# Kernel optimization log

Measured on AMD Instinct MI355X. Metric: run time of the kernel, lower is better.

The kernel has to match this reference:

```python
import jax, jax.numpy as jnp
import numpy as np

B, N, L, C = 4, 16, 192, 64
H = 128
ROW, COL = 16, 12  # L == ROW*COL, ROW >= COL
NUM = 2  # class_num


def setup_inputs() -> dict:
    key = jax.random.key(0)
    ks = jax.random.split(key, 12)
    s = 1.0 / np.sqrt(H).astype(np.float32)
    u = lambda k, shape: jax.random.uniform(k, shape, jnp.float32, -s, s)
    return {
        "x": jax.random.normal(ks[0], (B, N, L, C), jnp.float32),
        "pad_mask": jnp.ones((B, N), jnp.bool_),
        "fc3_w": u(ks[1], (H, C)), "fc3_b": u(ks[2], (H,)),
        "fc4_w": u(ks[3], (H, H)), "fc4_b": u(ks[4], (H,)),
        "W_enc": u(ks[5], (NUM, 6 * H, 3 * H)), "B_enc": u(ks[6], (NUM, 6 * H)),
        "fc1_w": u(ks[7], (NUM, 1, H)), "fc1_b": u(ks[8], (NUM, 1)),
        "fc2_w": u(ks[9], (NUM, 1, H)), "fc2_b": u(ks[10], (NUM, 1)),
    }


def _witran_encoder(a, W, Bb):
    # a: [COL*BN, slice_len, H] diagonally-shifted input; W: [6H, 3H]; Bb: [6H]
    RBN, slice_len, _ = a.shape
    BN = RBN // COL
    R = COL  # Water2sea_slice_num (after permute(2,0,1,3), slices run over col)
    slice_ids = jnp.arange(RBN) // BN
    xs = jnp.transpose(a, (1, 0, 2))  # [slice_len, RBN, H]

    def step(carry, inp):
        h_row, h_col = carry
        x_s, s = inp
        g = jnp.concatenate([h_row, h_col, x_s], axis=-1) @ W.T  # [RBN, 6H]
        # torch adds bias only to first batch*(s+1) rows, and only while s < slice_num
        mask = (slice_ids <= s) & (s < R)
        g = g + jnp.where(mask[:, None], Bb, jnp.zeros((), g.dtype))
        sig = jax.nn.sigmoid(g[:, : 4 * H])
        th = jnp.tanh(g[:, 4 * H:])
        u_r, o_r, u_c, o_c = jnp.split(sig, 4, axis=-1)
        i_r, i_c = jnp.split(th, 2, axis=-1)
        h_row = jnp.tanh((1 - u_r) * h_row + u_r * i_r) * o_r
        h_col = jnp.tanh((1 - u_c) * h_col + u_c * i_c) * o_c
        # saved pieces (only valid for late s; we keep the last, which is always valid)
        loc = jnp.clip(s - ROW + 1, 0, R - 1)
        row_save = jax.lax.dynamic_slice_in_dim(h_row, loc * BN, BN, axis=0)
        col_save = h_col[(R - 1) * BN:, :]  # save BEFORE roll, as in torch
        h_col = jnp.roll(h_col, BN, axis=0)
        return (h_row, h_col), (row_save, col_save)

    h0 = jnp.zeros((RBN, H), a.dtype)
    (_, _), (row_saves, col_saves) = jax.lax.scan(
        step, (h0, h0), (xs, jnp.arange(slice_len)))
    # last entries == hidden_row_all[:, -1, -1, :], hidden_col_all[:, -1, -1, :]
    return row_saves[-1], col_saves[-1]  # each [BN, H]


def reference(x, pad_mask, fc3_w, fc3_b, fc4_w, fc4_b, W_enc, B_enc,
              fc1_w, fc1_b, fc2_w, fc2_b):
    Bn, Nn = x.shape[0], x.shape[1]
    h = jax.nn.relu(x @ fc3_w.T + fc3_b) @ fc4_w.T + fc4_b  # [B,N,L,H]
    xr = h.reshape(-1, ROW, COL, H)          # [BN, row, col, H]
    inp = jnp.transpose(xr, (2, 0, 1, 3))    # [col, BN, row, H]
    slice_len = COL + ROW - 1
    # diagonal 'water2sea' shift: transfer[r, :, r:r+ROW] = inp[r]
    padded = jnp.pad(inp, ((0, 0), (0, 0), (0, COL - 1), (0, 0)))
    transfer = jax.vmap(lambda t, r: jnp.roll(t, r, axis=1))(padded, jnp.arange(COL))
    a = transfer.reshape(COL * Bn * Nn, slice_len, H)

    def per_class(W, Bb, f1w, f1b, f2w, f2b):
        row_last, col_last = _witran_encoder(a, W, Bb)
        # torch: row := hidden_col_all tail, col := hidden_row_all tail
        out = 0.5 * (col_last @ f1w.T + f1b) + 0.5 * (row_last @ f2w.T + f2b)
        return out[:, 0]  # [BN]

    y = jax.vmap(per_class)(W_enc, B_enc, fc1_w, fc1_b, fc2_w, fc2_b)  # [NUM, BN]
    return jnp.transpose(y).reshape(Bn, Nn, NUM)
```

## Files before the change

### kernel.cpp

```cpp
#include <hip/hip_runtime.h>

typedef _Float16 hf;
typedef _Float16 half2v __attribute__((ext_vector_type(2)));
typedef _Float16 half8 __attribute__((ext_vector_type(8)));
typedef float f32x4 __attribute__((ext_vector_type(4)));
typedef int int4v __attribute__((ext_vector_type(4)));

constexpr int Steps = 27;

constexpr int OFF_WX = 393216;
constexpr int OFF_F3 = 589824;
constexpr int OFF_F4 = 598016;
constexpr int OFF_XW = 614400;

__device__ __forceinline__ int aidx(int r, int k) {
  int blk = k >> 3;
  return r * 256 + (((blk ^ (r & 7)) & 31) << 3) + (k & 7);
}
__device__ __forceinline__ int hidx(int r, int k) {
  int blk = k >> 3;
  return r * 128 + (((blk ^ (r & 15)) & 15) << 3) + (k & 7);
}
__device__ __forceinline__ int xidx(int r, int k) {
  int blk = k >> 3;
  return r * 64 + (((blk ^ (r & 7)) & 7) << 3) + (k & 7);
}
__device__ __forceinline__ float rcpf_(float x) { return __builtin_amdgcn_rcpf(x); }
__device__ __forceinline__ float sigmoidf_(float x) { return rcpf_(1.0f + __expf(-x)); }
__device__ __forceinline__ float tanh_(float x) { return 1.0f - 2.0f * rcpf_(__expf(2.0f * x) + 1.0f); }

__device__ __forceinline__ void bar_lgkm() {
  __builtin_amdgcn_sched_barrier(0);
  asm volatile("s_waitcnt lgkmcnt(0)");
  __builtin_amdgcn_s_barrier();
  __builtin_amdgcn_sched_barrier(0);
}

__global__ __launch_bounds__(512) void prep(const float* __restrict__ fc3_w,
                                            const float* __restrict__ fc4_w,
                                            const float* __restrict__ W_enc,
                                            hf* __restrict__ wsh) {
  int idx = blockIdx.x * 512 + threadIdx.x;
  if (idx >= OFF_XW) return;
  float v;
  if (idx < OFF_WX) {
    int jj = idx & 7, lane = (idx >> 3) & 63, rest = idx >> 9;
    int ks = rest & 7; rest >>= 3;
    int j = rest % 3; rest /= 3;
    int wv = rest & 15, cls = rest >> 4;
    int gate = (wv < 8) ? (j < 2 ? j : 4) : (j < 2 ? j + 2 : 5);
    int n = gate * 128 + (wv & 7) * 16 + (lane & 15);
    int k = ks * 32 + ((lane >> 4) << 3) + jj;
    v = W_enc[(cls * 768 + n) * 384 + k];
  } else if (idx < OFF_F3) {
    int f = idx - OFF_WX;
    int j = f & 7, lane = (f >> 3) & 63, rest = f >> 9;
    int ks = rest & 3; rest >>= 2;
    int wv = rest & 7; rest >>= 3;
    int gate = rest % 6, cls = rest / 6;
    int n = gate * 128 + wv * 16 + (lane & 15);
    int k = 256 + ks * 32 + ((lane >> 4) << 3) + j;
    v = W_enc[(cls * 768 + n) * 384 + k];
  } else if (idx < OFF_F4) {
    int f = idx - OFF_F3;
    int j = f & 7, lane = (f >> 3) & 63, rest = f >> 9;
    int ks = rest & 1, wv = rest >> 1;
    int n = wv * 16 + (lane & 15), k = ks * 32 + ((lane >> 4) << 3) + j;
    v = fc3_w[n * 64 + k];
  } else {
    int f = idx - OFF_F4;
    int j = f & 7, lane = (f >> 3) & 63, rest = f >> 9;
    int ks = rest & 3, wv = rest >> 2;
    int n = wv * 16 + (lane & 15), k = ks * 32 + ((lane >> 4) << 3) + j;
    v = fc4_w[n * 128 + k];
  }
  wsh[idx] = (hf)v;
}

__global__ __launch_bounds__(512) void prelude(
    const float* __restrict__ x, const float* __restrict__ fc3_b, const float* __restrict__ fc4_b,
    const float* __restrict__ B_enc, const hf* __restrict__ wsh, hf* __restrict__ xWb) {
  const int t = threadIdx.x, lane = t & 63, wv = t >> 6;
  const int c16 = lane & 15, quad = lane >> 4;
  const int row0 = blockIdx.x * 64, bn = row0 / 192, l0 = row0 % 192;
  const int d = wv * 16 + c16;

  __shared__ __attribute__((aligned(16))) hf xA[64 * 64];
  __shared__ __attribute__((aligned(16))) hf hbuf[64 * 128];
  __shared__ __attribute__((aligned(16))) hf xout[64 * 768];
  __shared__ float actf[64];

  {
    int r = t >> 3, cb = (t & 7) * 8;
    const float* xp = x + (size_t)(row0 + r) * 64 + cb;
    f32x4 a = *(const f32x4*)xp, b = *(const f32x4*)(xp + 4);
    half8 h;
    h[0] = (hf)a.x; h[1] = (hf)a.y; h[2] = (hf)a.z; h[3] = (hf)a.w;
    h[4] = (hf)b.x; h[5] = (hf)b.y; h[6] = (hf)b.z; h[7] = (hf)b.w;
    *(half8*)&xA[xidx(r, cb)] = h;
  }
  if (t < 64) {
    int l = l0 + t;
    actf[t] = ((l / 12) + (l % 12)) < 12 ? 1.f : 0.f;
  }
  __syncthreads();

  {
    float b3v = fc3_b[d];
    half8 w0 = *(const half8*)(wsh + OFF_F3 + (wv * 2 + 0) * 512 + lane * 8);
    half8 w1 = *(const half8*)(wsh + OFF_F3 + (wv * 2 + 1) * 512 + lane * 8);
    f32x4 acc[4] = {{0, 0, 0, 0}, {0, 0, 0, 0}, {0, 0, 0, 0}, {0, 0, 0, 0}};
#pragma unroll
    for (int mt = 0; mt < 4; ++mt) {
      half8 a0 = *(const half8*)&xA[xidx(mt * 16 + c16, quad * 8)];
      half8 a1 = *(const half8*)&xA[xidx(mt * 16 + c16, 32 + quad * 8)];
      acc[mt] = __builtin_amdgcn_mfma_f32_16x16x32_f16(a0, w0, acc[mt], 0, 0, 0);
      acc[mt] = __builtin_amdgcn_mfma_f32_16x16x32_f16(a1, w1, acc[mt], 0, 0, 0);
    }
#pragma unroll
    for (int mt = 0; mt < 4; ++mt)
#pragma unroll
      for (int r = 0; r < 4; ++r)
        hbuf[hidx(mt * 16 + quad * 4 + r, d)] = (hf)fmaxf(acc[mt][r] + b3v, 0.f);
  }
  __syncthreads();

  {
    float b4v = fc4_b[d];
    half8 w4[4];
#pragma unroll
    for (int ks = 0; ks < 4; ++ks)
      w4[ks] = *(const half8*)(wsh + OFF_F4 + (wv * 4 + ks) * 512 + lane * 8);
    f32x4 acc[4] = {{0, 0, 0, 0}, {0, 0, 0, 0}, {0, 0, 0, 0}, {0, 0, 0, 0}};
#pragma unroll
    for (int mt = 0; mt < 4; ++mt)
#pragma unroll
      for (int ks = 0; ks < 4; ++ks) {
        half8 a = *(const half8*)&hbuf[hidx(mt * 16 + c16, ks * 32 + quad * 8)];
        acc[mt] = __builtin_amdgcn_mfma_f32_16x16x32_f16(a, w4[ks], acc[mt], 0, 0, 0);
      }
    __syncthreads();
#pragma unroll
    for (int mt = 0; mt < 4; ++mt)
#pragma unroll
      for (int r = 0; r < 4; ++r)
        hbuf[hidx(mt * 16 + quad * 4 + r, d)] = (hf)(acc[mt][r] + b4v);
  }
  __syncthreads();

  half8 af[4][4];
#pragma unroll
  for (int mt = 0; mt < 4; ++mt)
#pragma unroll
    for (int ks = 0; ks < 4; ++ks)
      af[mt][ks] = *(const half8*)&hbuf[hidx(mt * 16 + c16, ks * 32 + quad * 8)];

  for (int cls = 0; cls < 2; ++cls) {
    for (int g = 0; g < 6; ++g) {
      int pos = (g < 2) ? g : (g < 4 ? g + 1 : (g == 4 ? 2 : 5));
      half8 wf[4];
#pragma unroll
      for (int ks = 0; ks < 4; ++ks)
        wf[ks] = *(const half8*)(wsh + OFF_WX + (((cls * 6 + g) * 8 + wv) * 4 + ks) * 512 + lane * 8);
      float bv = B_enc[cls * 768 + g * 128 + d];
#pragma unroll
      for (int mt = 0; mt < 4; ++mt) {
        f32x4 acc = {0.f, 0.f, 0.f, 0.f};
#pragma unroll
        for (int ks = 0; ks < 4; ++ks)
          acc = __builtin_amdgcn_mfma_f32_16x16x32_f16(af[mt][ks], wf[ks], acc, 0, 0, 0);
#pragma unroll
        for (int r = 0; r < 4; ++r) {
          int row = mt * 16 + quad * 4 + r;
          xout[row * 768 + d * 6 + pos] = (hf)(acc[r] + actf[row] * bv);
        }
      }
    }
    __syncthreads();
    {
      const int* src = (const int*)xout;
      int* dst = (int*)(xWb + (((size_t)cls * 64 + bn) * 192 + l0) * 768);
#pragma unroll
      for (int i = 0; i < 12; ++i) {
        int base = (t + i * 512) * 4;
        *(int4v*)&dst[base] = *(const int4v*)&src[base];
      }
    }
    __syncthreads();
  }
}

__device__ __forceinline__ float lo16f(unsigned v) {
  return (float)__builtin_bit_cast(half2v, v)[0];
}
__device__ __forceinline__ float hi16f(unsigned v) {
  return (float)__builtin_bit_cast(half2v, v)[1];
}

__global__ __launch_bounds__(512, 2) __attribute__((amdgpu_waves_per_eu(2, 2))) void witran(
    const hf* __restrict__ wsh, const float* __restrict__ fc1_w, const float* __restrict__ fc1_b,
    const float* __restrict__ fc2_w, const float* __restrict__ fc2_b,
    const hf* __restrict__ xWb, float* __restrict__ out) {
  const int cls = blockIdx.x & 1, bn = blockIdx.x >> 1;
  const int t = threadIdx.x, lane = t & 63, wv = t >> 6;
  const int c16 = lane & 15, quad = lane >> 4;
  const int d = wv * 16 + c16;
  const bool act = (quad < 3);
  const int c0 = quad * 4;

  __shared__ __attribute__((aligned(16))) hf wlds[8 * 4096];
  __shared__ __attribute__((aligned(16))) hf A[2][4096];
  __shared__ float red[128];

  for (int i = t; i < 4096; i += 512) ((int*)A)[i] = 0;

  half8 wf[5][8];
  {
    const hf* wbR = wsh + ((size_t)((cls * 16 + wv) * 3) * 8) * 512 + lane * 8;
    const hf* wbC = wsh + ((size_t)((cls * 16 + 8 + wv) * 3) * 8) * 512 + lane * 8;
#pragma unroll
    for (int j = 0; j < 3; ++j)
#pragma unroll
      for (int ks = 0; ks < 8; ++ks)
        wf[j][ks] = *(const half8*)(wbR + (j * 8 + ks) * 512);
#pragma unroll
    for (int j = 0; j < 2; ++j)
#pragma unroll
      for (int ks = 0; ks < 8; ++ks)
        wf[3 + j][ks] = *(const half8*)(wbC + (j * 8 + ks) * 512);
#pragma unroll
    for (int ks = 0; ks < 8; ++ks)
      *(half8*)&wlds[wv * 4096 + ks * 512 + lane * 8] = *(const half8*)(wbC + (16 + ks) * 512);
  }

  const hf* xg = xWb + ((size_t)cls * 64 + bn) * 192 * 768;
  int xrun = d * 12 - c0 * 16896;
  unsigned pxc[4][3];
  float hr[4] = {0.f, 0.f, 0.f, 0.f};

  auto xload = [&](int s) {
#pragma unroll
    for (int r = 0; r < 4; ++r) {
      int c = c0 + r;
      bool ok = act && ((unsigned)(s - c) < 16u);
      int off = ok ? (xrun - r * 16896) : 0;
      const hf* p = (const hf*)((const char*)xg + off);
      pxc[r][0] = *(const unsigned*)p;
      pxc[r][1] = *(const unsigned*)(p + 2);
      pxc[r][2] = *(const unsigned*)(p + 4);
    }
    xrun += 18432;
  };

  auto step = [&](const hf* Ac, hf* An, int s) {
    float hcold[4];
#pragma unroll
    for (int r = 0; r < 4; ++r) hcold[r] = (float)Ac[aidx(c0 + r, 128 + d)];
    f32x4 acc[6];
#pragma unroll
    for (int g = 0; g < 6; ++g) acc[g] = (f32x4){0.f, 0.f, 0.f, 0.f};
#pragma unroll
    for (int ks = 0; ks < 8; ++ks) {
      half8 av = *(const half8*)&Ac[aidx(c16, ks * 32 + quad * 8)];
#pragma unroll
      for (int g = 0; g < 5; ++g)
        acc[g] = __builtin_amdgcn_mfma_f32_16x16x32_f16(av, wf[g][ks], acc[g], 0, 0, 0);
      half8 w5 = *(const half8*)&wlds[wv * 4096 + ks * 512 + lane * 8];
      acc[5] = __builtin_amdgcn_mfma_f32_16x16x32_f16(av, w5, acc[5], 0, 0, 0);
    }
    if (act) {
#pragma unroll
      for (int r = 0; r < 4; ++r) {
        int c = c0 + r;
        bool okx = ((unsigned)(s - c) < 16u);
        unsigned v0 = okx ? pxc[r][0] : 0u;
        unsigned v1 = okx ? pxc[r][1] : 0u;
        unsigned v2 = okx ? pxc[r][2] : 0u;
        float xur = lo16f(v0), xor_ = hi16f(v0);
        float xir = lo16f(v1), xuc = hi16f(v1);
        float xoc = lo16f(v2), xic = hi16f(v2);
        float uu = sigmoidf_(acc[0][r] + xur);
        float oo = sigmoidf_(acc[1][r] + xor_);
        float ii = tanh_(acc[2][r] + xir);
        float h1 = tanh_(hr[r] + uu * (ii - hr[r])) * oo;
        hr[r] = h1;
        An[aidx(c, d)] = (hf)h1;
        float u2 = sigmoidf_(acc[3][r] + xuc);
        float o2 = sigmoidf_(acc[4][r] + xoc);
        float i2 = tanh_(acc[5][r] + xic);
        float h2 = tanh_(hcold[r] + u2 * (i2 - hcold[r])) * o2;
        int cw = (c == 11) ? 0 : c + 1;
        An[aidx(cw, 128 + d)] = (hf)h2;
      }
    }
    xload(s + 1);
    bar_lgkm();
  };

  xload(0);
  bar_lgkm();

#pragma unroll 1
  for (int s = 0; s < Steps - 1; s += 2) {
    step(A[0], A[1], s);
    step(A[1], A[0], s + 1);
  }
  step(A[0], A[1], Steps - 1);

  const hf* Af = A[1];
  if (t < 128) {
    float hrv = (float)Af[aidx(11, t)];
    float hcv = (float)Af[aidx(0, 128 + t)];
    red[t] = 0.5f * (hcv * fc1_w[cls * 128 + t] + hrv * fc2_w[cls * 128 + t]);
  }
  __syncthreads();
  if (t == 0) {
    float sum = 0.f;
    for (int i = 0; i < 128; ++i) sum += red[i];
    out[bn * 2 + cls] = sum + 0.5f * (fc1_b[cls] + fc2_b[cls]);
  }
}

extern "C" void kernel_launch(void* const* d_in, const int* in_sizes, int n_in,
                              void* d_out, int out_size, void* d_ws, size_t ws_size,
                              hipStream_t stream) {
  const float* x = (const float*)d_in[0];
  const float* fc3_w = (const float*)d_in[2];
  const float* fc3_b = (const float*)d_in[3];
  const float* fc4_w = (const float*)d_in[4];
  const float* fc4_b = (const float*)d_in[5];
  const float* W_enc = (const float*)d_in[6];
  const float* B_enc = (const float*)d_in[7];
  const float* fc1_w = (const float*)d_in[8];
  const float* fc1_b = (const float*)d_in[9];
  const float* fc2_w = (const float*)d_in[10];
  const float* fc2_b = (const float*)d_in[11];
  float* out = (float*)d_out;

  hf* wsh = (hf*)d_ws;
  hf* xWb = wsh + OFF_XW;

  prep<<<dim3(1200), dim3(512), 0, stream>>>(fc3_w, fc4_w, W_enc, wsh);
  prelude<<<dim3(192), dim3(512), 0, stream>>>(x, fc3_b, fc4_b, B_enc, wsh, xWb);
  witran<<<dim3(128), dim3(512), 0, stream>>>(wsh, fc1_w, fc1_b, fc2_w, fc2_b, xWb, out);
}
```

Before: 161.7 us.

## Drop weight prep kernel and gather fp32 weights directly; halve prelude tile

Removes the separate prep kernel that reformatted fc3, fc4 and W_enc into fp16 MFMA-fragment layout. Each consumer kernel now loads fp32 weights straight from the original tensors and converts them in registers. The prelude tile shrinks from 64 to 32 rows, doubling its grid to 384 blocks for better CU coverage. This saves one launch and one pass over the weights, but the per-thread fp32 loads are strided and less coalesced, and weight bytes are re-read by more blocks.

```diff
diff --git a/kernel.cpp b/kernel.cpp
--- a/kernel.cpp
+++ b/kernel.cpp
@@ -2,16 +2,12 @@
 
 typedef _Float16 hf;
 typedef _Float16 half2v __attribute__((ext_vector_type(2)));
+typedef _Float16 half4 __attribute__((ext_vector_type(4)));
 typedef _Float16 half8 __attribute__((ext_vector_type(8)));
 typedef float f32x4 __attribute__((ext_vector_type(4)));
 typedef int int4v __attribute__((ext_vector_type(4)));
 
 constexpr int Steps = 27;
-
-constexpr int OFF_WX = 393216;
-constexpr int OFF_F3 = 589824;
-constexpr int OFF_F4 = 598016;
-constexpr int OFF_XW = 614400;
 
 __device__ __forceinline__ int aidx(int r, int k) {
   int blk = k >> 3;
@@ -36,70 +32,36 @@
   __builtin_amdgcn_sched_barrier(0);
 }
 
-__global__ __launch_bounds__(512) void prep(const float* __restrict__ fc3_w,
-                                            const float* __restrict__ fc4_w,
-                                            const float* __restrict__ W_enc,
-                                            hf* __restrict__ wsh) {
-  int idx = blockIdx.x * 512 + threadIdx.x;
-  if (idx >= OFF_XW) return;
-  float v;
-  if (idx < OFF_WX) {
-    int jj = idx & 7, lane = (idx >> 3) & 63, rest = idx >> 9;
-    int ks = rest & 7; rest >>= 3;
-    int j = rest % 3; rest /= 3;
-    int wv = rest & 15, cls = rest >> 4;
-    int gate = (wv < 8) ? (j < 2 ? j : 4) : (j < 2 ? j + 2 : 5);
-    int n = gate * 128 + (wv & 7) * 16 + (lane & 15);
-    int k = ks * 32 + ((lane >> 4) << 3) + jj;
-    v = W_enc[(cls * 768 + n) * 384 + k];
-  } else if (idx < OFF_F3) {
-    int f = idx - OFF_WX;
-    int j = f & 7, lane = (f >> 3) & 63, rest = f >> 9;
-    int ks = rest & 3; rest >>= 2;
-    int wv = rest & 7; rest >>= 3;
-    int gate = rest % 6, cls = rest / 6;
-    int n = gate * 128 + wv * 16 + (lane & 15);
-    int k = 256 + ks * 32 + ((lane >> 4) << 3) + j;
-    v = W_enc[(cls * 768 + n) * 384 + k];
-  } else if (idx < OFF_F4) {
-    int f = idx - OFF_F3;
-    int j = f & 7, lane = (f >> 3) & 63, rest = f >> 9;
-    int ks = rest & 1, wv = rest >> 1;
-    int n = wv * 16 + (lane & 15), k = ks * 32 + ((lane >> 4) << 3) + j;
-    v = fc3_w[n * 64 + k];
-  } else {
-    int f = idx - OFF_F4;
-    int j = f & 7, lane = (f >> 3) & 63, rest = f >> 9;
-    int ks = rest & 3, wv = rest >> 2;
-    int n = wv * 16 + (lane & 15), k = ks * 32 + ((lane >> 4) << 3) + j;
-    v = fc4_w[n * 128 + k];
-  }
-  wsh[idx] = (hf)v;
+__device__ __forceinline__ half8 gather8(const float* __restrict__ p) {
+  f32x4 a = *(const f32x4*)p, b = *(const f32x4*)(p + 4);
+  half8 h;
+  h[0] = (hf)a.x; h[1] = (hf)a.y; h[2] = (hf)a.z; h[3] = (hf)a.w;
+  h[4] = (hf)b.x; h[5] = (hf)b.y; h[6] = (hf)b.z; h[7] = (hf)b.w;
+  return h;
 }
 
 __global__ __launch_bounds__(512) void prelude(
-    const float* __restrict__ x, const float* __restrict__ fc3_b, const float* __restrict__ fc4_b,
-    const float* __restrict__ B_enc, const hf* __restrict__ wsh, hf* __restrict__ xWb) {
+    const float* __restrict__ x, const float* __restrict__ fc3_w, const float* __restrict__ fc3_b,
+    const float* __restrict__ fc4_w, const float* __restrict__ fc4_b,
+    const float* __restrict__ W_enc, const float* __restrict__ B_enc, hf* __restrict__ xWb) {
   const int t = threadIdx.x, lane = t & 63, wv = t >> 6;
   const int c16 = lane & 15, quad = lane >> 4;
-  const int row0 = blockIdx.x * 64, bn = row0 / 192, l0 = row0 % 192;
+  const int row0 = blockIdx.x * 32, bn = row0 / 192, l0 = row0 % 192;
   const int d = wv * 16 + c16;
 
-  __shared__ __attribute__((aligned(16))) hf xA[64 * 64];
-  __shared__ __attribute__((aligned(16))) hf hbuf[64 * 128];
-  __shared__ __attribute__((aligned(16))) hf xout[64 * 768];
-  __shared__ float actf[64];
+  __shared__ __attribute__((aligned(16))) hf xA[32 * 64];
+  __shared__ __attribute__((aligned(16))) hf hbuf[32 * 128];
+  __shared__ __attribute__((aligned(16))) hf xout[32 * 768];
+  __shared__ float actf[32];
 
   {
-    int r = t >> 3, cb = (t & 7) * 8;
-    const float* xp = x + (size_t)(row0 + r) * 64 + cb;
-    f32x4 a = *(const f32x4*)xp, b = *(const f32x4*)(xp + 4);
-    half8 h;
+    int r = t >> 4, cb = (t & 15) * 4;
+    f32x4 a = *(const f32x4*)(x + (size_t)(row0 + r) * 64 + cb);
+    half4 h;
     h[0] = (hf)a.x; h[1] = (hf)a.y; h[2] = (hf)a.z; h[3] = (hf)a.w;
-    h[4] = (hf)b.x; h[5] = (hf)b.y; h[6] = (hf)b.z; h[7] = (hf)b.w;
-    *(half8*)&xA[xidx(r, cb)] = h;
-  }
-  if (t < 64) {
+    *(half4*)&xA[xidx(r, cb)] = h;
+  }
+  if (t < 32) {
     int l = l0 + t;
     actf[t] = ((l / 12) + (l % 12)) < 12 ? 1.f : 0.f;
   }
@@ -107,18 +69,18 @@
 
   {
     float b3v = fc3_b[d];
-    half8 w0 = *(const half8*)(wsh + OFF_F3 + (wv * 2 + 0) * 512 + lane * 8);
-    half8 w1 = *(const half8*)(wsh + OFF_F3 + (wv * 2 + 1) * 512 + lane * 8);
-    f32x4 acc[4] = {{0, 0, 0, 0}, {0, 0, 0, 0}, {0, 0, 0, 0}, {0, 0, 0, 0}};
-#pragma unroll
-    for (int mt = 0; mt < 4; ++mt) {
+    half8 w0 = gather8(fc3_w + d * 64 + quad * 8);
+    half8 w1 = gather8(fc3_w + d * 64 + 32 + quad * 8);
+    f32x4 acc[2] = {{0, 0, 0, 0}, {0, 0, 0, 0}};
+#pragma unroll
+    for (int mt = 0; mt < 2; ++mt) {
       half8 a0 = *(const half8*)&xA[xidx(mt * 16 + c16, quad * 8)];
       half8 a1 = *(const half8*)&xA[xidx(mt * 16 + c16, 32 + quad * 8)];
       acc[mt] = __builtin_amdgcn_mfma_f32_16x16x32_f16(a0, w0, acc[mt], 0, 0, 0);
       acc[mt] = __builtin_amdgcn_mfma_f32_16x16x32_f16(a1, w1, acc[mt], 0, 0, 0);
     }
 #pragma unroll
-    for (int mt = 0; mt < 4; ++mt)
+    for (int mt = 0; mt < 2; ++mt)
 #pragma unroll
       for (int r = 0; r < 4; ++r)
         hbuf[hidx(mt * 16 + quad * 4 + r, d)] = (hf)fmaxf(acc[mt][r] + b3v, 0.f);
@@ -130,10 +92,10 @@
     half8 w4[4];
 #pragma unroll
     for (int ks = 0; ks < 4; ++ks)
-      w4[ks] = *(const half8*)(wsh + OFF_F4 + (wv * 4 + ks) * 512 + lane * 8);
-    f32x4 acc[4] = {{0, 0, 0, 0}, {0, 0, 0, 0}, {0, 0, 0, 0}, {0, 0, 0, 0}};
-#pragma unroll
-    for (int mt = 0; mt < 4; ++mt)
+      w4[ks] = gather8(fc4_w + d * 128 + ks * 32 + quad * 8);
+    f32x4 acc[2] = {{0, 0, 0, 0}, {0, 0, 0, 0}};
+#pragma unroll
+    for (int mt = 0; mt < 2; ++mt)
 #pragma unroll
       for (int ks = 0; ks < 4; ++ks) {
         half8 a = *(const half8*)&hbuf[hidx(mt * 16 + c16, ks * 32 + quad * 8)];
@@ -141,16 +103,16 @@
       }
     __syncthreads();
 #pragma unroll
-    for (int mt = 0; mt < 4; ++mt)
+    for (int mt = 0; mt < 2; ++mt)
 #pragma unroll
       for (int r = 0; r < 4; ++r)
         hbuf[hidx(mt * 16 + quad * 4 + r, d)] = (hf)(acc[mt][r] + b4v);
   }
   __syncthreads();
 
-  half8 af[4][4];
-#pragma unroll
-  for (int mt = 0; mt < 4; ++mt)
+  half8 af[2][4];
+#pragma unroll
+  for (int mt = 0; mt < 2; ++mt)
 #pragma unroll
     for (int ks = 0; ks < 4; ++ks)
       af[mt][ks] = *(const half8*)&hbuf[hidx(mt * 16 + c16, ks * 32 + quad * 8)];
@@ -158,17 +120,18 @@
   for (int cls = 0; cls < 2; ++cls) {
     for (int g = 0; g < 6; ++g) {
       int pos = (g < 2) ? g : (g < 4 ? g + 1 : (g == 4 ? 2 : 5));
-      half8 wf[4];
+      const float* wb = W_enc + (size_t)(cls * 768 + g * 128 + d) * 384 + 256;
+      half8 wfk[4];
 #pragma unroll
       for (int ks = 0; ks < 4; ++ks)
-        wf[ks] = *(const half8*)(wsh + OFF_WX + (((cls * 6 + g) * 8 + wv) * 4 + ks) * 512 + lane * 8);
+        wfk[ks] = gather8(wb + ks * 32 + quad * 8);
       float bv = B_enc[cls * 768 + g * 128 + d];
 #pragma unroll
-      for (int mt = 0; mt < 4; ++mt) {
+      for (int mt = 0; mt < 2; ++mt) {
         f32x4 acc = {0.f, 0.f, 0.f, 0.f};
 #pragma unroll
         for (int ks = 0; ks < 4; ++ks)
-          acc = __builtin_amdgcn_mfma_f32_16x16x32_f16(af[mt][ks], wf[ks], acc, 0, 0, 0);
+          acc = __builtin_amdgcn_mfma_f32_16x16x32_f16(af[mt][ks], wfk[ks], acc, 0, 0, 0);
 #pragma unroll
         for (int r = 0; r < 4; ++r) {
           int row = mt * 16 + quad * 4 + r;
@@ -181,7 +144,7 @@
       const int* src = (const int*)xout;
       int* dst = (int*)(xWb + (((size_t)cls * 64 + bn) * 192 + l0) * 768);
 #pragma unroll
-      for (int i = 0; i < 12; ++i) {
+      for (int i = 0; i < 6; ++i) {
         int base = (t + i * 512) * 4;
         *(int4v*)&dst[base] = *(const int4v*)&src[base];
       }
@@ -198,7 +161,7 @@
 }
 
 __global__ __launch_bounds__(512, 2) __attribute__((amdgpu_waves_per_eu(2, 2))) void witran(
-    const hf* __restrict__ wsh, const float* __restrict__ fc1_w, const float* __restrict__ fc1_b,
+    const float* __restrict__ W_enc, const float* __restrict__ fc1_w, const float* __restrict__ fc1_b,
     const float* __restrict__ fc2_w, const float* __restrict__ fc2_b,
     const hf* __restrict__ xWb, float* __restrict__ out) {
   const int cls = blockIdx.x & 1, bn = blockIdx.x >> 1;
@@ -216,21 +179,19 @@
 
   half8 wf[5][8];
   {
-    const hf* wbR = wsh + ((size_t)((cls * 16 + wv) * 3) * 8) * 512 + lane * 8;
-    const hf* wbC = wsh + ((size_t)((cls * 16 + 8 + wv) * 3) * 8) * 512 + lane * 8;
-#pragma unroll
-    for (int j = 0; j < 3; ++j)
+    const float* wc = W_enc + (size_t)cls * 768 * 384;
+    const int gates[5] = {0, 1, 4, 2, 3};
+#pragma unroll
+    for (int j = 0; j < 5; ++j) {
+      const float* base = wc + (size_t)(gates[j] * 128 + d) * 384;
 #pragma unroll
       for (int ks = 0; ks < 8; ++ks)
-        wf[j][ks] = *(const half8*)(wbR + (j * 8 + ks) * 512);
-#pragma unroll
-    for (int j = 0; j < 2; ++j)
-#pragma unroll
-      for (int ks = 0; ks < 8; ++ks)
-        wf[3 + j][ks] = *(const half8*)(wbC + (j * 8 + ks) * 512);
+        wf[j][ks] = gather8(base + ks * 32 + quad * 8);
+    }
+    const float* b5 = wc + (size_t)(5 * 128 + d) * 384;
 #pragma unroll
     for (int ks = 0; ks < 8; ++ks)
-      *(half8*)&wlds[wv * 4096 + ks * 512 + lane * 8] = *(const half8*)(wbC + (16 + ks) * 512);
+      *(half8*)&wlds[wv * 4096 + ks * 512 + lane * 8] = gather8(b5 + ks * 32 + quad * 8);
   }
 
   const hf* xg = xWb + ((size_t)cls * 64 + bn) * 192 * 768;
@@ -337,10 +298,8 @@
   const float* fc2_b = (const float*)d_in[11];
   float* out = (float*)d_out;
 
-  hf* wsh = (hf*)d_ws;
-  hf* xWb = wsh + OFF_XW;
-
-  prep<<<dim3(1200), dim3(512), 0, stream>>>(fc3_w, fc4_w, W_enc, wsh);
-  prelude<<<dim3(192), dim3(512), 0, stream>>>(x, fc3_b, fc4_b, B_enc, wsh, xWb);
-  witran<<<dim3(128), dim3(512), 0, stream>>>(wsh, fc1_w, fc1_b, fc2_w, fc2_b, xWb, out);
-}
+  hf* xWb = (hf*)d_ws;
+
+  prelude<<<dim3(384), dim3(512), 0, stream>>>(x, fc3_w, fc3_b, fc4_w, fc4_b, W_enc, B_enc, xWb);
+  witran<<<dim3(128), dim3(512), 0, stream>>>(W_enc, fc1_w, fc1_b, fc2_w, fc2_b, xWb, out);
+}
```

Measured after the change: 211.5 us. +30.8%, slower.
